# Kernel tuning notes

Measured on AMD Instinct MI355X. Metric: run time of the kernel, lower is better.

Reference implementation:

```python
import jax, jax.numpy as jnp
import numpy as np

SHIFT = 1  # fixed shift_direction (original picks +-1 randomly at init)


def setup_inputs() -> dict:
    key = jax.random.key(0)
    kx, kw = jax.random.split(key)
    x = jax.random.normal(kx, (128, 256, 28, 28), dtype=jnp.float32)
    W = jax.random.normal(kw, (32, 3, 4, 3, 8), dtype=jnp.float32)
    return {"x": x, "W": W}


def reference(x, W):
    # (128,256,28,28) -> (128,2,128,28,28) -> sum over dim 1 -> (128,128,28,28)
    t = x.reshape(128, 2, 128, 28, 28).sum(axis=1)
    # split channels into 32 groups of 4: (n, i=32, m=4, h=28, w=28)
    t = t.reshape(128, 32, 4, 28, 28)
    # first unfold: kernel (3,1), pad (1,0) over the i=32 axis -> neighbor stack j in {-1,0,+1}
    tp = jnp.pad(t, ((0, 0), (1, 1), (0, 0), (0, 0), (0, 0)))
    t3 = jnp.stack([tp[:, 0:32], tp[:, 1:33], tp[:, 2:34]], axis=1)  # (n, j3, i32, m, h, w)
    # cyclic shift along w
    t3 = jnp.roll(t3, SHIFT, axis=5)
    # second unfold: kernel (3,1), pad (1,0) over the w axis -> neighbor stack kw in {-1,0,+1}
    tp2 = jnp.pad(t3, ((0, 0), (0, 0), (0, 0), (0, 0), (0, 0), (1, 1)))
    t3 = jnp.stack([tp2[..., 0:28], tp2[..., 1:29], tp2[..., 2:30]], axis=5)  # (n, j3, i32, m, h, kw, w)
    # contraction: einsum labels match torch 'njimpol,jimlk->njpok' after its permute.
    # Our t3 dims (n, i_e=3, j_e=32, m=4, p=h, l=kw, o=w); W dims (j=32, i=3, m=4, l=3, k=8)
    out = jnp.einsum('nijmplo,jimlk->njpok', t3, W)  # (128, 32, 28, 28, 8)
    out = out.transpose(0, 2, 3, 1, 4).reshape(128, 28, 28, 256)
    out = jnp.roll(out, SHIFT, axis=1)
    return out.transpose(0, 3, 1, 2)  # (128, 256, 28, 28)
```

## Files before the change

kernel.cpp:

```cpp
#include <hip/hip_runtime.h>

typedef float __attribute__((ext_vector_type(4))) f32x4;
typedef unsigned int u32;
typedef u32 __attribute__((ext_vector_type(4))) u32x4;


__device__ __forceinline__ u32 pack2bf(float lo, float hi) {
    u32 a = __float_as_uint(lo), b = __float_as_uint(hi);
    a = (a + 0x7FFFu + ((a >> 16) & 1u)) >> 16;
    b = (b + 0x7FFFu + ((b >> 16) & 1u)) >> 16;
    return a | (b << 16);
}

__device__ __forceinline__ float dot2bf(u32 t2, u32 w2, float acc) {
    asm("v_dot2_f32_bf16 %0, %1, %2, %0" : "+v"(acc) : "v"(t2), "v"(w2));
    return acc;
}

__global__ __launch_bounds__(1024, 8) void fused_shift_conv(
    const float* __restrict__ x, const float* __restrict__ Wt, float* __restrict__ out)
{
    __shared__ __align__(16) u32 L[8192];

    const int tid = threadIdx.x;
    const int blk = blockIdx.x;
    const int n   = blk / 7;
    const int b4  = blk - n * 7;
    const int h0  = b4 * 4;

    const float* xn = x + (size_t)n * 200704;

    #pragma unroll
    for (int rd = 0; rd < 2; ++rd) {
        const int f = tid + rd * 1024;
        if (f < 1792) {
            const int p   = f / 28;
            const int rem = f - p * 28;
            const int row = rem / 7;
            const int q   = rem - row * 7;
            int hs = h0 - 1 + row;
            hs = hs < 0 ? 27 : hs;
            const float* b0 = xn + (2 * p) * 784 + hs * 28 + q * 4;
            const f32x4 l0 = *(const f32x4*)b0;
            const f32x4 l1 = *(const f32x4*)(b0 + 784);
            const f32x4 u0 = *(const f32x4*)(b0 + 100352);
            const f32x4 u1 = *(const f32x4*)(b0 + 784 + 100352);
            const f32x4 s0 = l0 + u0, s1 = l1 + u1;
            u32x4 wv;
            #pragma unroll
            for (int e = 0; e < 4; ++e) wv[e] = pack2bf(s0[e], s1[e]);
            const int sw = (p >> 1) & 7;
            *(u32x4*)&L[row * 2048 + p * 32 + (((q ^ sw)) << 2)] = wv;
        }
    }

    const int t  = tid & 255;
    const int s_ = tid >> 8;
    const int j = t >> 3, k = t & 7;
    u32 w2[3][2][3];
    {
        const float* wp = Wt + j * 288 + k;
        #pragma unroll
        for (int a = 0; a < 3; ++a)
            #pragma unroll
            for (int m2 = 0; m2 < 2; ++m2)
                #pragma unroll
                for (int bb = 0; bb < 3; ++bb)
                    w2[a][m2][bb] = pack2bf(wp[a*96 + (2*m2  )*24 + bb*8],
                                            wp[a*96 + (2*m2+1)*24 + bb*8]);
    }
    if (j == 0) {
        #pragma unroll
        for (int m2 = 0; m2 < 2; ++m2)
            #pragma unroll
            for (int bb = 0; bb < 3; ++bb) w2[0][m2][bb] = 0u;
    }
    if (j == 31) {
        #pragma unroll
        for (int m2 = 0; m2 < 2; ++m2)
            #pragma unroll
            for (int bb = 0; bb < 3; ++bb) w2[2][m2][bb] = 0u;
    }

    __syncthreads();

    const u32* Bs = L + s_ * 2048;
    float acc[28];
    #pragma unroll
    for (int w = 0; w < 28; ++w) acc[w] = 0.f;

    #pragma unroll
    for (int a = 0; a < 3; ++a) {
        int g = j + a - 1;
        g = g < 0 ? 0 : (g > 31 ? 31 : g);
        const int s = g & 7;
        #pragma unroll
        for (int m2 = 0; m2 < 2; ++m2) {
            const int rowd = (g * 2 + m2) * 32;
            const u32 t2 = w2[a][m2][2], t1 = w2[a][m2][1], t0 = w2[a][m2][0];
            #pragma unroll
            for (int qb = 0; qb < 7; ++qb) {
                const u32x4 v = *(const u32x4*)&Bs[rowd + ((qb ^ s) << 2)];
                #pragma unroll
                for (int e = 0; e < 4; ++e) {
                    const int wp_ = qb * 4 + e;
                    if (wp_ != 27) acc[wp_] = dot2bf(v[e], t2, acc[wp_]);
                    acc[(wp_ + 1) % 28] = dot2bf(v[e], t1, acc[(wp_ + 1) % 28]);
                    if (wp_ != 26) acc[(wp_ + 2) % 28] = dot2bf(v[e], t0, acc[(wp_ + 2) % 28]);
                }
            }
        }
    }

    float* Lf = (float*)L;
    float* outn = out + (size_t)n * 200704;
    #pragma unroll
    for (int c = 0; c < 4; ++c) {
        __syncthreads();
        if ((j >> 3) == c) {
            const int oc = (j & 7) * 8 + k;
            float* dst = Lf + oc * 116 + s_ * 28;
            #pragma unroll
            for (int qq = 0; qq < 7; ++qq) {
                f32x4 o;
                o.x = acc[qq * 4 + 0];
                o.y = acc[qq * 4 + 1];
                o.z = acc[qq * 4 + 2];
                o.w = acc[qq * 4 + 3];
                *(f32x4*)(dst + qq * 4) = o;
            }
        }
        __syncthreads();
        #pragma unroll
        for (int rd = 0; rd < 2; ++rd) {
            const int fo = tid + rd * 1024;
            if (fo < 1792) {
                const int chl = fo / 28;
                const int rem = fo - chl * 28;
                const f32x4 v = *(const f32x4*)(Lf + chl * 116 + rem * 4);
                *(f32x4*)(outn + (size_t)(c * 64 + chl) * 784 + h0 * 28 + rem * 4) = v;
            }
        }
    }
}

extern "C" void kernel_launch(void* const* d_in, const int* in_sizes, int n_in,
                              void* d_out, int out_size, void* d_ws, size_t ws_size,
                              hipStream_t stream) {
    const float* x  = (const float*)d_in[0];
    const float* Wt = (const float*)d_in[1];
    float* out      = (float*)d_out;

    const int nbatch = in_sizes[0] / 200704;
    fused_shift_conv<<<nbatch * 7, 1024, 0, stream>>>(x, Wt, out);
}
```

Measured before the change: 54.09 us.

## Split each block to one output row with 256 threads instead of four rows

Each block now computes a single output row for one batch item, using 256 threads and 28 blocks per image instead of 1024 threads covering four rows. LDS use per block drops to a quarter, which is meant to improve occupancy and scheduling granularity and to lower the cost of block-wide barriers. The output staging switches to a 29-float channel stride. In exchange, global reads and writes become shorter 112-byte row segments instead of contiguous four-row chunks, and each block reloads and repacks the weights. The 29-float stride also means the 16-byte LDS vector accesses are no longer 16-byte aligned.

Measured after the change: 63.32 us. 1.17x slower.

```diff
diff --git a/kernel.cpp b/kernel.cpp
--- a/kernel.cpp
+++ b/kernel.cpp
@@ -17,30 +17,26 @@
     return acc;
 }
 
-__global__ __launch_bounds__(1024, 8) void fused_shift_conv(
+__global__ __launch_bounds__(256, 8) void fused_shift_conv(
     const float* __restrict__ x, const float* __restrict__ Wt, float* __restrict__ out)
 {
-    __shared__ __align__(16) u32 L[8192];
+    __shared__ __align__(16) u32 L[2048];
 
     const int tid = threadIdx.x;
-    const int blk = blockIdx.x;
-    const int n   = blk / 7;
-    const int b4  = blk - n * 7;
-    const int h0  = b4 * 4;
+    const int R   = blockIdx.x;
+    const int n   = R / 28;
+    const int h   = R - n * 28;
+    const int h_src = (h + 27) % 28;
 
-    const float* xn = x + (size_t)n * 200704;
+    const float* xn = x + (size_t)n * 200704 + h_src * 28;
 
     #pragma unroll
-    for (int rd = 0; rd < 2; ++rd) {
-        const int f = tid + rd * 1024;
-        if (f < 1792) {
-            const int p   = f / 28;
-            const int rem = f - p * 28;
-            const int row = rem / 7;
-            const int q   = rem - row * 7;
-            int hs = h0 - 1 + row;
-            hs = hs < 0 ? 27 : hs;
-            const float* b0 = xn + (2 * p) * 784 + hs * 28 + q * 4;
+    for (int it = 0; it < 2; ++it) {
+        const int f = tid + it * 256;
+        if (f < 448) {
+            const int p = f / 7;
+            const int q = f - p * 7;
+            const float* b0 = xn + (2 * p) * 784 + q * 4;
             const f32x4 l0 = *(const f32x4*)b0;
             const f32x4 l1 = *(const f32x4*)(b0 + 784);
             const f32x4 u0 = *(const f32x4*)(b0 + 100352);
@@ -50,13 +46,11 @@
             #pragma unroll
             for (int e = 0; e < 4; ++e) wv[e] = pack2bf(s0[e], s1[e]);
             const int sw = (p >> 1) & 7;
-            *(u32x4*)&L[row * 2048 + p * 32 + (((q ^ sw)) << 2)] = wv;
+            *(u32x4*)&L[p * 32 + ((q ^ sw) << 2)] = wv;
         }
     }
 
-    const int t  = tid & 255;
-    const int s_ = tid >> 8;
-    const int j = t >> 3, k = t & 7;
+    const int j = tid >> 3, k = tid & 7;
     u32 w2[3][2][3];
     {
         const float* wp = Wt + j * 288 + k;
@@ -82,9 +76,14 @@
             for (int bb = 0; bb < 3; ++bb) w2[2][m2][bb] = 0u;
     }
 
+    const int f0 = tid;
+    const int c0 = f0 / 7, q0 = f0 - c0 * 7;
+    const int f1 = tid + 256;
+    const int c1 = f1 / 7, q1 = f1 - c1 * 7;
+    const bool has1 = (f1 < 448);
+
     __syncthreads();
 
-    const u32* Bs = L + s_ * 2048;
     float acc[28];
     #pragma unroll
     for (int w = 0; w < 28; ++w) acc[w] = 0.f;
@@ -100,7 +99,7 @@
             const u32 t2 = w2[a][m2][2], t1 = w2[a][m2][1], t0 = w2[a][m2][0];
             #pragma unroll
             for (int qb = 0; qb < 7; ++qb) {
-                const u32x4 v = *(const u32x4*)&Bs[rowd + ((qb ^ s) << 2)];
+                const u32x4 v = *(const u32x4*)&L[rowd + ((qb ^ s) << 2)];
                 #pragma unroll
                 for (int e = 0; e < 4; ++e) {
                     const int wp_ = qb * 4 + e;
@@ -113,13 +112,12 @@
     }
 
     float* Lf = (float*)L;
-    float* outn = out + (size_t)n * 200704;
+    float* outn = out + (size_t)n * 200704 + h * 28;
     #pragma unroll
     for (int c = 0; c < 4; ++c) {
         __syncthreads();
-        if ((j >> 3) == c) {
-            const int oc = (j & 7) * 8 + k;
-            float* dst = Lf + oc * 116 + s_ * 28;
+        if ((tid >> 6) == c) {
+            float* dst = Lf + (tid & 63) * 29;
             #pragma unroll
             for (int qq = 0; qq < 7; ++qq) {
                 f32x4 o;
@@ -131,15 +129,13 @@
             }
         }
         __syncthreads();
-        #pragma unroll
-        for (int rd = 0; rd < 2; ++rd) {
-            const int fo = tid + rd * 1024;
-            if (fo < 1792) {
-                const int chl = fo / 28;
-                const int rem = fo - chl * 28;
-                const f32x4 v = *(const f32x4*)(Lf + chl * 116 + rem * 4);
-                *(f32x4*)(outn + (size_t)(c * 64 + chl) * 784 + h0 * 28 + rem * 4) = v;
-            }
+        {
+            const f32x4 v = *(const f32x4*)(Lf + c0 * 29 + q0 * 4);
+            *(f32x4*)(outn + (size_t)(c * 64 + c0) * 784 + q0 * 4) = v;
+        }
+        if (has1) {
+            const f32x4 v = *(const f32x4*)(Lf + c1 * 29 + q1 * 4);
+            *(f32x4*)(outn + (size_t)(c * 64 + c1) * 784 + q1 * 4) = v;
         }
     }
 }
@@ -152,5 +148,5 @@
     float* out      = (float*)d_out;
 
     const int nbatch = in_sizes[0] / 200704;
-    fused_shift_conv<<<nbatch * 7, 1024, 0, stream>>>(x, Wt, out);
+    fused_shift_conv<<<nbatch * 28, 256, 0, stream>>>(x, Wt, out);
 }
```
